# Kernel optimization log

Measured on AMD Instinct MI355X. Metric: run time of the kernel, lower is better.

The kernel has to match this reference:

```python
import jax, jax.numpy as jnp
import numpy as np

CHANNELS = 128
NUM_HEADS = 4
NUM_GROUPS = 32
EPS = 1e-5


def setup_inputs() -> dict:
    key = jax.random.key(0)
    ks = jax.random.split(key, 7)
    C = CHANNELS
    x = jax.random.normal(ks[0], (2, C, 64, 64), dtype=jnp.float32)
    norm_w = jnp.ones((C,), jnp.float32)
    norm_b = jnp.zeros((C,), jnp.float32)
    qkv_w = jax.random.normal(ks[1], (3 * C, C), jnp.float32) * (1.0 / np.sqrt(C))
    qkv_b = jax.random.normal(ks[2], (3 * C,), jnp.float32) * 0.01
    proj_w = jax.random.normal(ks[3], (C, C), jnp.float32) * (1.0 / np.sqrt(C))
    proj_b = jax.random.normal(ks[4], (C,), jnp.float32) * 0.01
    return {"x": x, "norm_w": norm_w, "norm_b": norm_b,
            "qkv_w": qkv_w, "qkv_b": qkv_b,
            "proj_w": proj_w, "proj_b": proj_b}


def group_norm(x, w, b):
    B, C, H, W = x.shape
    g = NUM_GROUPS
    xg = x.reshape(B, g, C // g, H, W)
    mean = xg.mean(axis=(2, 3, 4), keepdims=True)
    var = xg.var(axis=(2, 3, 4), keepdims=True)
    xg = (xg - mean) * jax.lax.rsqrt(var + EPS)
    x = xg.reshape(B, C, H, W)
    return x * w[None, :, None, None] + b[None, :, None, None]


def reference(x, norm_w, norm_b, qkv_w, qkv_b, proj_w, proj_b):
    B, C, H, W = x.shape
    nh = NUM_HEADS
    dh = C // nh
    scale = dh ** (-0.5)
    residual = x
    h = group_norm(x, norm_w, norm_b)
    # 1x1 conv == channel matmul: [B,3C,H,W]
    qkv = jnp.einsum('bchw,oc->bohw', h, qkv_w) + qkv_b[None, :, None, None]
    qkv = qkv.reshape(B, 3, nh, dh, H * W)
    q, k, v = qkv[:, 0], qkv[:, 1], qkv[:, 2]  # [B, nh, dh, HW]
    # attention over spatial tokens: attn[b,h,s,t]
    attn = jnp.einsum('bhds,bhdt->bhst', q, k) * scale
    attn = jax.nn.softmax(attn, axis=-1)
    out = jnp.einsum('bhst,bhdt->bhds', attn, v)  # [B, nh, dh, HW]
    out = out.reshape(B, C, H, W)
    out = jnp.einsum('bchw,oc->bohw', out, proj_w) + proj_b[None, :, None, None]
    return out + residual
```

## Files before the change

kernel.cpp:

```cpp
#include <hip/hip_runtime.h>
#include <stdint.h>

#define S_TOT 4096
#define CH 128
#define NH 4
#define DH 32

typedef __attribute__((ext_vector_type(4))) float f32x4;
typedef __attribute__((ext_vector_type(8))) short s16x8;

__device__ __forceinline__ unsigned short f2bf(float f){
  union { float f; unsigned u; } v; v.f = f;
  unsigned r = v.u + 0x7fffu + ((v.u >> 16) & 1u);
  return (unsigned short)(r >> 16);
}
__device__ __forceinline__ unsigned pk2(float a, float b){
  return (unsigned)f2bf(a) | ((unsigned)f2bf(b) << 16);
}
__device__ __forceinline__ unsigned cvtpk(float a, float b){
  unsigned r;
  asm("v_cvt_pk_bf16_f32 %0, %1, %2" : "=v"(r) : "v"(a), "v"(b));
  return r;
}
__device__ __forceinline__ float bf2f(unsigned short u){
  union { unsigned u; float f; } v; v.u = ((unsigned)u) << 16;
  return v.f;
}
__device__ __forceinline__ void g2l16(const unsigned short* g, unsigned short* l){
  __builtin_amdgcn_global_load_lds(
      (__attribute__((address_space(1))) void*)const_cast<unsigned short*>(g),
      (__attribute__((address_space(3))) void*)l, 16, 0, 0);
}

__global__ void k_pre(const float* __restrict__ x, float* __restrict__ stats,
                      const float* __restrict__ qkvw, const float* __restrict__ projw,
                      unsigned short* __restrict__ wq, unsigned short* __restrict__ wp){
  if (blockIdx.x >= 64){
    int i = (blockIdx.x - 64) * 256 + threadIdx.x;
    if (i < 384*128) wq[i] = f2bf(qkvw[i]);
    int j = i - 384*128;
    if (j >= 0 && j < 128*128) wp[j] = f2bf(projw[j]);
    return;
  }
  int bg = blockIdx.x;
  const float4* p = (const float4*)(x + (size_t)bg * 16384);
  float s = 0.f, ss = 0.f;
  #pragma unroll
  for (int i = 0; i < 16; ++i){
    float4 v = p[threadIdx.x + i*256];
    s  += v.x + v.y + v.z + v.w;
    ss += v.x*v.x + v.y*v.y + v.z*v.z + v.w*v.w;
  }
  #pragma unroll
  for (int m = 1; m < 64; m <<= 1){ s += __shfl_xor(s, m); ss += __shfl_xor(ss, m); }
  __shared__ float red[8];
  int wid = threadIdx.x >> 6;
  if ((threadIdx.x & 63) == 0){ red[wid*2] = s; red[wid*2+1] = ss; }
  __syncthreads();
  if (threadIdx.x == 0){
    float S = red[0]+red[2]+red[4]+red[6], SS = red[1]+red[3]+red[5]+red[7];
    float mean = S * (1.f/16384.f);
    float var  = SS * (1.f/16384.f) - mean*mean;
    stats[bg*2]   = mean;
    stats[bg*2+1] = rsqrtf(var + 1e-5f);
  }
}

__global__ void k_gnapply(const float* __restrict__ x, const float* __restrict__ stats,
                          const float* __restrict__ nw, const float* __restrict__ nb,
                          unsigned short* __restrict__ hT){
  __shared__ float lds[64*129];
  int b  = blockIdx.x >> 6;
  int s0 = (blockIdx.x & 63) * 64;
  int sid = threadIdx.x & 63, cg = threadIdx.x >> 6;
  #pragma unroll 4
  for (int c4 = 0; c4 < 32; ++c4){
    int c = c4*4 + cg;
    float mean = stats[(b*32 + c4)*2], rstd = stats[(b*32 + c4)*2 + 1];
    float v = x[((size_t)(b*CH + c))*S_TOT + s0 + sid];
    v = (v - mean) * rstd * nw[c] + nb[c];
    lds[sid*129 + c] = v;
  }
  __syncthreads();
  int row = threadIdx.x >> 2, q = threadIdx.x & 3, c0 = q*32;
  unsigned short* dst = hT + ((size_t)(b*S_TOT) + s0 + row) * CH + c0;
  const float* src = lds + row*129 + c0;
  #pragma unroll
  for (int cc = 0; cc < 4; ++cc){
    uint4 w;
    w.x = pk2(src[cc*8+0], src[cc*8+1]);
    w.y = pk2(src[cc*8+2], src[cc*8+3]);
    w.z = pk2(src[cc*8+4], src[cc*8+5]);
    w.w = pk2(src[cc*8+6], src[cc*8+7]);
    *(uint4*)(dst + cc*8) = w;
  }
}

__global__ void k_qkv(const unsigned short* __restrict__ hT, const unsigned short* __restrict__ wq,
                      const float* __restrict__ qkvb,
                      unsigned short* __restrict__ qT, unsigned short* __restrict__ kv){
  const float SC = 0.17677669529663687f * 1.4426950408889634f;
  int lane = threadIdx.x & 63, wid = threadIdx.x >> 6;
  int lo = lane & 15, hi = lane >> 4;
  int b  = blockIdx.z;
  int o0 = blockIdx.y * 64 + wid * 16;
  int sb = blockIdx.x * 64;
  s16x8 af[4];
  #pragma unroll
  for (int kk = 0; kk < 4; ++kk)
    af[kk] = *(const s16x8*)(wq + (size_t)(o0+lo)*CH + kk*32 + hi*8);
  #pragma unroll
  for (int st = 0; st < 4; ++st){
    int s0 = sb + st*16;
    const unsigned short* hrow = hT + ((size_t)(b*S_TOT) + s0 + lo) * CH + hi*8;
    f32x4 acc = {0.f,0.f,0.f,0.f};
    #pragma unroll
    for (int kk = 0; kk < 4; ++kk){
      s16x8 bfr = *(const s16x8*)(hrow + kk*32);
      acc = __builtin_amdgcn_mfma_f32_16x16x32_bf16(af[kk], bfr, acc, 0, 0, 0);
    }
    int s = s0 + lo;
    #pragma unroll
    for (int r = 0; r < 4; ++r){
      int o = o0 + hi*4 + r;
      float val = acc[r] + qkvb[o];
      if (o < 128){
        int h = o >> 5, d = o & 31;
        qT[(((size_t)(b*NH + h))*S_TOT + s)*DH + d] = f2bf(val * SC);
      } else if (o < 256){
        int o2 = o - 128, h = o2 >> 5, d = o2 & 31;
        kv[(((size_t)(b*NH + h)*128 + (s >> 5)) << 11) + ((s & 31) << 5) + d] = f2bf(val);
      } else {
        int o3 = o - 256, h = o3 >> 5, d = o3 & 31;
        int pos = s & 31;
        int hi2 = (pos & 15) >> 2;
        int j2  = (pos & 3) + ((pos & 16) ? 4 : 0);
        kv[(((size_t)(b*NH + h)*128 + (s >> 5)) << 11) + 1024 + (d << 5) + hi2*8 + j2] = f2bf(val);
      }
    }
  }
}

__global__ void __launch_bounds__(256) k_attn(const unsigned short* __restrict__ qT,
                                              const unsigned short* __restrict__ kv,
                                              unsigned short* __restrict__ po,
                                              float* __restrict__ ls){
  __shared__ __align__(16) unsigned short smem[8192];
  int lane = threadIdx.x & 63;
  int wid = threadIdx.x >> 6;
  int lo = lane & 15, hi = lane >> 4;
  int bh = blockIdx.x & 7;
  int sp = blockIdx.x >> 3;
  int sw = blockIdx.y * 128 + wid * 32;
  int tb = sp * 16;
  const unsigned short* qh = qT + (size_t)bh * S_TOT * DH;
  const unsigned short* kvbase = kv + (((size_t)bh*128 + tb) << 11);

  s16x8 qf0 = *(const s16x8*)(qh + (size_t)(sw + lo)*DH + hi*8);
  s16x8 qf1 = *(const s16x8*)(qh + (size_t)(sw + 16 + lo)*DH + hi*8);
  const f32x4 z = {0.f,0.f,0.f,0.f};
  f32x4 acc00 = z, acc01 = z, acc10 = z, acc11 = z, accL0 = z, accL1 = z;
  s16x8 onesf;
  #pragma unroll
  for (int i = 0; i < 8; ++i) onesf[i] = (short)0x3F80;

  auto compute = [&](const s16x8& kf0, const s16x8& kf1, const s16x8& vf0, const s16x8& vf1){
    __builtin_amdgcn_s_setprio(1);
    f32x4 p0 = __builtin_amdgcn_mfma_f32_16x16x32_bf16(kf0, qf0, z, 0, 0, 0);
    f32x4 p1 = __builtin_amdgcn_mfma_f32_16x16x32_bf16(kf1, qf0, z, 0, 0, 0);
    f32x4 r0 = __builtin_amdgcn_mfma_f32_16x16x32_bf16(kf0, qf1, z, 0, 0, 0);
    f32x4 r1 = __builtin_amdgcn_mfma_f32_16x16x32_bf16(kf1, qf1, z, 0, 0, 0);
    #pragma unroll
    for (int r = 0; r < 4; ++r){
      p0[r] = __builtin_amdgcn_exp2f(p0[r]);
      p1[r] = __builtin_amdgcn_exp2f(p1[r]);
      r0[r] = __builtin_amdgcn_exp2f(r0[r]);
      r1[r] = __builtin_amdgcn_exp2f(r1[r]);
    }
    union { unsigned u[4]; s16x8 v; } pa0, pa1;
    pa0.u[0] = cvtpk(p0[0],p0[1]); pa0.u[1] = cvtpk(p0[2],p0[3]);
    pa0.u[2] = cvtpk(p1[0],p1[1]); pa0.u[3] = cvtpk(p1[2],p1[3]);
    pa1.u[0] = cvtpk(r0[0],r0[1]); pa1.u[1] = cvtpk(r0[2],r0[3]);
    pa1.u[2] = cvtpk(r1[0],r1[1]); pa1.u[3] = cvtpk(r1[2],r1[3]);
    acc00 = __builtin_amdgcn_mfma_f32_16x16x32_bf16(pa0.v, vf0, acc00, 0, 0, 0);
    acc01 = __builtin_amdgcn_mfma_f32_16x16x32_bf16(pa0.v, vf1, acc01, 0, 0, 0);
    acc10 = __builtin_amdgcn_mfma_f32_16x16x32_bf16(pa1.v, vf0, acc10, 0, 0, 0);
    acc11 = __builtin_amdgcn_mfma_f32_16x16x32_bf16(pa1.v, vf1, acc11, 0, 0, 0);
    accL0 = __builtin_amdgcn_mfma_f32_16x16x32_bf16(pa0.v, onesf, accL0, 0, 0, 0);
    accL1 = __builtin_amdgcn_mfma_f32_16x16x32_bf16(pa1.v, onesf, accL1, 0, 0, 0);
    __builtin_amdgcn_s_setprio(0);
  };

  {
    const unsigned short* g = kvbase + wid*1024 + lane*8;
    unsigned short* l = smem + wid*1024;
    g2l16(g, l);
    g2l16(g + 512, l + 512);
  }
  __syncthreads();

  int buf = 0;
  for (int grp = 0; grp < 8; ++grp){
    int gn = (grp < 7) ? grp + 1 : 7;
    const unsigned short* g = kvbase + gn*4096 + wid*1024 + lane*8;
    unsigned short* l = smem + (buf^1)*4096 + wid*1024;
    g2l16(g, l);
    g2l16(g + 512, l + 512);
    const unsigned short* lb = smem + buf*4096 + (lo << 5) + hi*8;
    #pragma unroll
    for (int t = 0; t < 2; ++t){
      const unsigned short* tl = lb + t*2048;
      s16x8 kf0 = *(const s16x8*)(tl);
      s16x8 kf1 = *(const s16x8*)(tl + 512);
      s16x8 vf0 = *(const s16x8*)(tl + 1024);
      s16x8 vf1 = *(const s16x8*)(tl + 1536);
      compute(kf0, kf1, vf0, vf1);
    }
    __syncthreads();
    buf ^= 1;
  }

  unsigned short* pob = po + (size_t)(bh*8 + sp) * S_TOT * DH;
  float* lsb = ls + (size_t)(bh*8 + sp) * S_TOT;
  #pragma unroll
  for (int r = 0; r < 4; ++r){
    int s0r = sw + hi*4 + r;
    pob[(size_t)s0r*DH + lo]      = f2bf(acc00[r]);
    pob[(size_t)s0r*DH + lo + 16] = f2bf(acc01[r]);
    int s1r = sw + 16 + hi*4 + r;
    pob[(size_t)s1r*DH + lo]      = f2bf(acc10[r]);
    pob[(size_t)s1r*DH + lo + 16] = f2bf(acc11[r]);
  }
  if (lo == 0){
    #pragma unroll
    for (int r = 0; r < 4; ++r){
      lsb[sw + hi*4 + r]      = accL0[r];
      lsb[sw + 16 + hi*4 + r] = accL1[r];
    }
  }
}

__global__ void k_comb(const unsigned short* __restrict__ po, const float* __restrict__ ls,
                       unsigned short* __restrict__ aoT){
  int t = blockIdx.x * 256 + threadIdx.x;
  int d4 = (t & 7) * 4;
  int s  = (t >> 3) & 4095;
  int bh = t >> 15;
  float l = 0.f;
  float4 v = {0.f,0.f,0.f,0.f};
  #pragma unroll
  for (int sp = 0; sp < 8; ++sp){
    size_t base = (size_t)(bh*8 + sp) * S_TOT + s;
    l += ls[base];
    ushort4 pv = *(const ushort4*)(po + base*DH + d4);
    v.x += bf2f(pv.x); v.y += bf2f(pv.y); v.z += bf2f(pv.z); v.w += bf2f(pv.w);
  }
  float inv = 1.f / l;
  ushort4 o;
  o.x = f2bf(v.x * inv); o.y = f2bf(v.y * inv);
  o.z = f2bf(v.z * inv); o.w = f2bf(v.w * inv);
  *(ushort4*)(aoT + ((size_t)(bh*4096 + s))*DH + d4) = o;
}

__global__ void k_proj(const unsigned short* __restrict__ aoT, const unsigned short* __restrict__ wp,
                       const float* __restrict__ pb, const float* __restrict__ x,
                       float* __restrict__ out){
  int lane = threadIdx.x & 63, wid = threadIdx.x >> 6;
  int lo = lane & 15, hi = lane >> 4;
  int b  = blockIdx.z;
  int o0 = blockIdx.y * 64 + wid * 16;
  int sb = blockIdx.x * 64;
  s16x8 af[4];
  #pragma unroll
  for (int kk = 0; kk < 4; ++kk)
    af[kk] = *(const s16x8*)(wp + (size_t)(o0+lo)*CH + kk*32 + hi*8);
  #pragma unroll
  for (int st = 0; st < 4; ++st){
    int s0 = sb + st*16;
    f32x4 acc = {0.f,0.f,0.f,0.f};
    #pragma unroll
    for (int kk = 0; kk < 4; ++kk){
      s16x8 bfr = *(const s16x8*)(aoT + (((size_t)(b*NH + kk))*S_TOT + s0 + lo)*DH + hi*8);
      acc = __builtin_amdgcn_mfma_f32_16x16x32_bf16(af[kk], bfr, acc, 0, 0, 0);
    }
    #pragma unroll
    for (int r = 0; r < 4; ++r){
      int o = o0 + hi*4 + r;
      size_t idx = ((size_t)(b*CH + o))*S_TOT + s0 + lo;
      out[idx] = acc[r] + pb[o] + x[idx];
    }
  }
}

extern "C" void kernel_launch(void* const* d_in, const int* in_sizes, int n_in,
                              void* d_out, int out_size, void* d_ws, size_t ws_size,
                              hipStream_t stream){
  const float* x     = (const float*)d_in[0];
  const float* nw    = (const float*)d_in[1];
  const float* nb    = (const float*)d_in[2];
  const float* qkvw  = (const float*)d_in[3];
  const float* qkvb  = (const float*)d_in[4];
  const float* projw = (const float*)d_in[5];
  const float* projb = (const float*)d_in[6];
  float* out = (float*)d_out;
  char* ws = (char*)d_ws;
  const size_t MB = 1048576;
  unsigned short* qT  = (unsigned short*)(ws);
  unsigned short* kv  = (unsigned short*)(ws + 2*MB);
  unsigned short* aoT = (unsigned short*)(ws + 6*MB);
  unsigned short* wq  = (unsigned short*)(ws + 8*MB);
  unsigned short* wp  = (unsigned short*)(ws + 8*MB + 131072);
  float* stats        = (float*)(ws + 8*MB + 196608);
  float* ls           = (float*)(ws + 8*MB + 262144);
  unsigned short* hT  = (unsigned short*)(ws + 10*MB);
  unsigned short* po  = (unsigned short*)(ws + 12*MB);

  hipLaunchKernelGGL(k_pre,     dim3(320),      dim3(256), 0, stream, x, stats, qkvw, projw, wq, wp);
  hipLaunchKernelGGL(k_gnapply, dim3(128),      dim3(256), 0, stream, x, stats, nw, nb, hT);
  hipLaunchKernelGGL(k_qkv,     dim3(64, 6, 2), dim3(256), 0, stream, hT, wq, qkvb, qT, kv);
  hipLaunchKernelGGL(k_attn,    dim3(64, 32),   dim3(256), 0, stream, qT, kv, po, ls);
  hipLaunchKernelGGL(k_comb,    dim3(1024),     dim3(256), 0, stream, po, ls, aoT);
  hipLaunchKernelGGL(k_proj,    dim3(64, 2, 2), dim3(256), 0, stream, aoT, wp, projb, x, out);
}
```

Baseline: 67.98 us.

## Fuse split-attention combine into projection kernel and skip redundant last prefetch

Removes the separate combine kernel by merging the eight split-KV partial outputs and normalizing by the summed row-sums directly inside the projection kernel, feeding the result straight into MFMA as the B operand. Each projection block now computes all 128 output channels so the combine work is done once per spatial tile. This drops one launch and the aoT round-trip through global memory, but the projection grid shrinks to 128 blocks, each doing more serial loads. The attention loop also skips the redundant final prefetch.

```diff
diff --git a/kernel.cpp b/kernel.cpp
--- a/kernel.cpp
+++ b/kernel.cpp
@@ -201,11 +201,12 @@
 
   int buf = 0;
   for (int grp = 0; grp < 8; ++grp){
-    int gn = (grp < 7) ? grp + 1 : 7;
-    const unsigned short* g = kvbase + gn*4096 + wid*1024 + lane*8;
-    unsigned short* l = smem + (buf^1)*4096 + wid*1024;
-    g2l16(g, l);
-    g2l16(g + 512, l + 512);
+    if (grp < 7){
+      const unsigned short* g = kvbase + (grp + 1)*4096 + wid*1024 + lane*8;
+      unsigned short* l = smem + (buf^1)*4096 + wid*1024;
+      g2l16(g, l);
+      g2l16(g + 512, l + 512);
+    }
     const unsigned short* lb = smem + buf*4096 + (lo << 5) + hi*8;
     #pragma unroll
     for (int t = 0; t < 2; ++t){
@@ -240,54 +241,56 @@
   }
 }
 
-__global__ void k_comb(const unsigned short* __restrict__ po, const float* __restrict__ ls,
-                       unsigned short* __restrict__ aoT){
-  int t = blockIdx.x * 256 + threadIdx.x;
-  int d4 = (t & 7) * 4;
-  int s  = (t >> 3) & 4095;
-  int bh = t >> 15;
-  float l = 0.f;
-  float4 v = {0.f,0.f,0.f,0.f};
-  #pragma unroll
-  for (int sp = 0; sp < 8; ++sp){
-    size_t base = (size_t)(bh*8 + sp) * S_TOT + s;
-    l += ls[base];
-    ushort4 pv = *(const ushort4*)(po + base*DH + d4);
-    v.x += bf2f(pv.x); v.y += bf2f(pv.y); v.z += bf2f(pv.z); v.w += bf2f(pv.w);
-  }
-  float inv = 1.f / l;
-  ushort4 o;
-  o.x = f2bf(v.x * inv); o.y = f2bf(v.y * inv);
-  o.z = f2bf(v.z * inv); o.w = f2bf(v.w * inv);
-  *(ushort4*)(aoT + ((size_t)(bh*4096 + s))*DH + d4) = o;
-}
-
-__global__ void k_proj(const unsigned short* __restrict__ aoT, const unsigned short* __restrict__ wp,
+__global__ void k_proj(const unsigned short* __restrict__ po, const float* __restrict__ ls,
+                       const unsigned short* __restrict__ wp,
                        const float* __restrict__ pb, const float* __restrict__ x,
                        float* __restrict__ out){
   int lane = threadIdx.x & 63, wid = threadIdx.x >> 6;
   int lo = lane & 15, hi = lane >> 4;
-  int b  = blockIdx.z;
-  int o0 = blockIdx.y * 64 + wid * 16;
+  int b  = blockIdx.y;
   int sb = blockIdx.x * 64;
-  s16x8 af[4];
-  #pragma unroll
-  for (int kk = 0; kk < 4; ++kk)
-    af[kk] = *(const s16x8*)(wp + (size_t)(o0+lo)*CH + kk*32 + hi*8);
+  int o0a = wid * 16, o0b = o0a + 64;
+  s16x8 afa[4], afb[4];
+  #pragma unroll
+  for (int kk = 0; kk < 4; ++kk){
+    afa[kk] = *(const s16x8*)(wp + (size_t)(o0a+lo)*CH + kk*32 + hi*8);
+    afb[kk] = *(const s16x8*)(wp + (size_t)(o0b+lo)*CH + kk*32 + hi*8);
+  }
   #pragma unroll
   for (int st = 0; st < 4; ++st){
-    int s0 = sb + st*16;
-    f32x4 acc = {0.f,0.f,0.f,0.f};
+    int s = sb + st*16 + lo;
+    f32x4 acca = {0.f,0.f,0.f,0.f}, accb = {0.f,0.f,0.f,0.f};
     #pragma unroll
     for (int kk = 0; kk < 4; ++kk){
-      s16x8 bfr = *(const s16x8*)(aoT + (((size_t)(b*NH + kk))*S_TOT + s0 + lo)*DH + hi*8);
-      acc = __builtin_amdgcn_mfma_f32_16x16x32_bf16(af[kk], bfr, acc, 0, 0, 0);
+      int bh = b*NH + kk;
+      float l = 0.f;
+      float v0=0.f,v1=0.f,v2=0.f,v3=0.f,v4=0.f,v5=0.f,v6=0.f,v7=0.f;
+      #pragma unroll
+      for (int sp = 0; sp < 8; ++sp){
+        size_t base = (size_t)(bh*8 + sp) * S_TOT + s;
+        l += ls[base];
+        ushort4 pv0 = *(const ushort4*)(po + base*DH + hi*8);
+        ushort4 pv1 = *(const ushort4*)(po + base*DH + hi*8 + 4);
+        v0 += bf2f(pv0.x); v1 += bf2f(pv0.y); v2 += bf2f(pv0.z); v3 += bf2f(pv0.w);
+        v4 += bf2f(pv1.x); v5 += bf2f(pv1.y); v6 += bf2f(pv1.z); v7 += bf2f(pv1.w);
+      }
+      float inv = 1.f / l;
+      union { unsigned u[4]; s16x8 v; } bfr;
+      bfr.u[0] = pk2(v0*inv, v1*inv);
+      bfr.u[1] = pk2(v2*inv, v3*inv);
+      bfr.u[2] = pk2(v4*inv, v5*inv);
+      bfr.u[3] = pk2(v6*inv, v7*inv);
+      acca = __builtin_amdgcn_mfma_f32_16x16x32_bf16(afa[kk], bfr.v, acca, 0, 0, 0);
+      accb = __builtin_amdgcn_mfma_f32_16x16x32_bf16(afb[kk], bfr.v, accb, 0, 0, 0);
     }
     #pragma unroll
     for (int r = 0; r < 4; ++r){
-      int o = o0 + hi*4 + r;
-      size_t idx = ((size_t)(b*CH + o))*S_TOT + s0 + lo;
-      out[idx] = acc[r] + pb[o] + x[idx];
+      int oa = o0a + hi*4 + r;
+      size_t idxa = ((size_t)(b*CH + oa))*S_TOT + s;
+      out[idxa] = acca[r] + pb[oa] + x[idxa];
+      int ob = o0b + hi*4 + r;
+      size_t idxb = ((size_t)(b*CH + ob))*S_TOT + s;
+      out[idxb] = accb[r] + pb[ob] + x[idxb];
     }
   }
 }
@@ -307,7 +310,6 @@
   const size_t MB = 1048576;
   unsigned short* qT  = (unsigned short*)(ws);
   unsigned short* kv  = (unsigned short*)(ws + 2*MB);
-  unsigned short* aoT = (unsigned short*)(ws + 6*MB);
   unsigned short* wq  = (unsigned short*)(ws + 8*MB);
   unsigned short* wp  = (unsigned short*)(ws + 8*MB + 131072);
   float* stats        = (float*)(ws + 8*MB + 196608);
@@ -319,6 +321,5 @@
   hipLaunchKernelGGL(k_gnapply, dim3(128),      dim3(256), 0, stream, x, stats, nw, nb, hT);
   hipLaunchKernelGGL(k_qkv,     dim3(64, 6, 2), dim3(256), 0, stream, hT, wq, qkvb, qT, kv);
   hipLaunchKernelGGL(k_attn,    dim3(64, 32),   dim3(256), 0, stream, qT, kv, po, ls);
-  hipLaunchKernelGGL(k_comb,    dim3(1024),     dim3(256), 0, stream, po, ls, aoT);
-  hipLaunchKernelGGL(k_proj,    dim3(64, 2, 2), dim3(256), 0, stream, aoT, wp, projb, x, out);
-}
+  hipLaunchKernelGGL(k_proj,    dim3(64, 2),    dim3(256), 0, stream, po, ls, wp, projb, x, out);
+}
```

Measured after the change: 103.8 us. +52.8%, slower.
